# Optimization experiments

Measured on AMD Instinct MI355X. Metric: run time of the kernel, lower is better.

## Reference

```python
import jax, jax.numpy as jnp
import numpy as np

N = 50000        # num nodes
F = 64           # feature_size
G = 64           # graph_embedding_size
C = 4            # num_edge_cat
NNZ = 800000     # edges per category
L0 = 128         # first MLP hidden layer
EMB = 64         # embedding_size
EPS = 1e-5


def _glorot(key, shape):
    fan_in, fan_out = shape[-2], shape[-1]
    lim = jnp.sqrt(6.0 / (fan_in + fan_out))
    return jax.random.uniform(key, shape, jnp.float32, -lim, lim)


def setup_inputs() -> dict:
    key = jax.random.key(0)
    ks = jax.random.split(key, 8)
    A = jax.random.randint(ks[0], (C, 2, NNZ), 0, N, dtype=jnp.int64)
    X = jax.random.normal(ks[1], (N, F), jnp.float32)
    Ws = _glorot(ks[2], (C, F, G))            # per-edge-cat projection
    W0 = _glorot(ks[3], (C * G, L0))          # Linear0 weight (in,out)
    b0 = jnp.zeros((L0,), jnp.float32)
    gamma = jnp.ones((L0,), jnp.float32)      # BatchNorm1d weight
    beta = jnp.zeros((L0,), jnp.float32)      # BatchNorm1d bias
    W1 = _glorot(ks[4], (L0, EMB))            # Linear1 weight (in,out)
    b1 = jnp.zeros((EMB,), jnp.float32)
    return {"A": A, "X": X, "Ws": Ws, "W0": W0, "b0": b0,
            "gamma": gamma, "beta": beta, "W1": W1, "b1": b1,
            "mini_batch": 0}


def reference(A, X, Ws, W0, b0, gamma, beta, W1, b1, mini_batch):
    # mini_batch == False path. Instead of materializing dense NxN adjacency,
    # aggregate directly over edge lists (same math: (E @ X)[i] = sum_{(i,j) in E} X[j]).
    n = X.shape[0]
    XW = jnp.einsum('nf,cfg->cng', X, Ws)                       # [C,N,G]
    def agg(edges, xw):                                          # edges [2,nnz], xw [N,G]
        return jax.ops.segment_sum(xw[edges[1]], edges[0], num_segments=n)
    H = jax.vmap(agg)(A, XW)                                     # [C,N,G]
    H = jnp.transpose(H, (1, 0, 2)).reshape(n, -1)               # concat over edge cats -> [N, C*G]
    # NodeEmbedding: Linear -> BatchNorm1d (training stats) -> ELU -> Linear
    h = H @ W0 + b0
    mean = jnp.mean(h, axis=0)
    var = jnp.mean((h - mean) ** 2, axis=0)                      # biased var, as torch BN
    h = (h - mean) * jax.lax.rsqrt(var + EPS) * gamma + beta
    h = jax.nn.elu(h)
    return h @ W1 + b1                                           # [N, EMB]
```

## Files before the change

kernel.cpp:

```cpp
#include <hip/hip_runtime.h>
#include <hip/hip_bf16.h>

#define NN    50000
#define CC    4
#define NNZV  800000
#define TOTE  (CC * NNZV)
#define NWG   1024
#define EPW   (TOTE / NWG)
#define NFB   782
#define NPART 8
#define RCAPV 768
#define BCAP  (NPART * RCAPV)
#define NRB   782
#define NXB   782

using bf16 = __hip_bfloat16;
typedef short short8 __attribute__((ext_vector_type(8)));
typedef float f32x4  __attribute__((ext_vector_type(4)));
typedef unsigned short u16x8 __attribute__((ext_vector_type(8)));

__device__ __forceinline__ float bfu2f(unsigned short u) {
    union { unsigned int i; float f; } v;
    v.i = ((unsigned int)u) << 16;
    return v.f;
}
__device__ __forceinline__ float cvt(float x) { return x; }
__device__ __forceinline__ float cvt(bf16 x)  { return __bfloat162float(x); }
__device__ __forceinline__ unsigned short tobits(float x) {
    bf16 t = __float2bfloat16(x);
    return *(unsigned short*)&t;
}

__device__ __forceinline__ void detect_flags(const unsigned int* __restrict__ Xw,
                                             const unsigned int* __restrict__ Aw,
                                             int* dcnt, int& f32f, int& i64f) {
    const int t = threadIdx.x, nthr = blockDim.x;
    if (t < 2) dcnt[t] = 0;
    __syncthreads();
    int c1 = 0;
    for (int i = t; i < 1024; i += nthr) {
        unsigned b = (Xw[i] >> 7) & 0xFF;
        if (b >= 118 && b <= 134) c1++;
    }
    if (c1) atomicAdd(&dcnt[0], c1);
    if (t < 128) { if (Aw[2 * t + 1] == 0) atomicAdd(&dcnt[1], 1); }
    __syncthreads();
    f32f = (dcnt[0] < 512) ? 1 : 0;
    i64f = (dcnt[1] >= 96) ? 1 : 0;
    __syncthreads();
}

template<typename TF>
__device__ __forceinline__ void pack_body(const TF* __restrict__ W0, const TF* __restrict__ W1,
                                          const TF* __restrict__ Ws, const TF* __restrict__ b0,
                                          const TF* __restrict__ b1,
                                          unsigned short* __restrict__ Wb,
                                          unsigned short* __restrict__ Wb1,
                                          float* __restrict__ bias0, float* __restrict__ bias1,
                                          int trip) {
    const int lane = trip & 63;
    const int q = lane >> 4, cI = lane & 15;
    if (trip < 4096) {
        const int k0 = trip >> 9, t8 = (trip >> 6) & 7;
        const int kbase = k0 * 32 + q * 8;
        const int col   = t8 * 16 + cI;
        const int c     = kbase >> 6;
        float w0c[64];
        #pragma unroll
        for (int g = 0; g < 64; ++g)
            w0c[g] = cvt(W0[(size_t)(c * 64 + g) * 128 + col]);
        #pragma unroll
        for (int j = 0; j < 8; ++j) {
            const int f = (kbase + j) & 63;
            const TF* wsrow = Ws + ((size_t)c * 64 + f) * 64;
            float acc = 0.f;
            #pragma unroll
            for (int g = 0; g < 64; ++g)
                acc += cvt(wsrow[g]) * w0c[g];
            Wb[(size_t)trip * 8 + j] = tobits(acc);
        }
    } else if (trip < 5120) {
        const int u = trip - 4096;
        const int k0 = u >> 8, t4 = (u >> 6) & 3;
        #pragma unroll
        for (int j = 0; j < 8; ++j)
            Wb1[(size_t)u * 8 + j] =
                tobits(cvt(W1[(size_t)(k0 * 32 + q * 8 + j) * 64 + t4 * 16 + cI]));
    } else if (trip < 5248) {
        bias0[trip - 5120] = cvt(b0[trip - 5120]);
    } else if (trip < 5312) {
        bias1[trip - 5248] = cvt(b1[trip - 5248]);
    }
}

__global__ __launch_bounds__(256) void pack_kernel(const void* X, const void* A,
                                                   const void* W0, const void* W1,
                                                   const void* Ws, const void* b0,
                                                   const void* b1,
                                                   unsigned short* Wb, unsigned short* Wb1,
                                                   float* bias0, float* bias1,
                                                   unsigned int* zeroReg) {
    __shared__ int dcnt[2];
    int f32f, i64f;
    detect_flags((const unsigned int*)X, (const unsigned int*)A, dcnt, f32f, i64f);
    const int t = threadIdx.x;
    if (blockIdx.x == 0) {
        for (int i = t; i < 8448; i += 256) zeroReg[i] = 0u;
    }
    const int trip = blockIdx.x * 256 + t;
    if (trip >= 5312) return;
    if (f32f) pack_body<float>((const float*)W0, (const float*)W1, (const float*)Ws,
                               (const float*)b0, (const float*)b1, Wb, Wb1, bias0, bias1, trip);
    else      pack_body<bf16> ((const bf16*)W0, (const bf16*)W1, (const bf16*)Ws,
                               (const bf16*)b0, (const bf16*)b1, Wb, Wb1, bias0, bias1, trip);
}

template<typename TI>
__device__ __forceinline__ void cscat2_body(const TI* __restrict__ A,
                                            unsigned int* __restrict__ gcur,
                                            unsigned int* __restrict__ recs,
                                            unsigned int* lh, unsigned int* lrec) {
    const int w = blockIdx.x, t = threadIdx.x;
    const int v = w & (NPART - 1);
    #pragma unroll
    for (int u = 0; u < 4; ++u) lh[t + u * 256] = 0;
    __syncthreads();
    const int base   = w * EPW;
    const int c      = base / NNZV;
    const int eibase = base - c * NNZV;
    const TI* Ad = A + (size_t)(c * 2 + 0) * NNZV + eibase;
    const TI* As = A + (size_t)(c * 2 + 1) * NNZV + eibase;
    for (int i = t; i < EPW; i += 256) {
        const int dst = (int)Ad[i];
        const int src = (int)As[i];
        unsigned int rec = 0xFFFFFFFFu;
        if ((unsigned)dst < NN && (unsigned)src < NN) {
            rec = ((unsigned)dst << 16) | (unsigned)src;
            atomicAdd(&lh[dst >> 6], 1u);
        }
        lrec[i] = rec;
    }
    __syncthreads();
    unsigned int cl[4], sl[4];
    #pragma unroll
    for (int u = 0; u < 4; ++u) cl[u] = lh[t + u * 256];
    __syncthreads();
    #pragma unroll
    for (int u = 0; u < 4; ++u)
        sl[u] = cl[u] ? atomicAdd(&gcur[(v << 10) + t + u * 256], cl[u]) : 0u;
    #pragma unroll
    for (int u = 0; u < 4; ++u) lh[t + u * 256] = sl[u];
    __syncthreads();
    const unsigned int cb = (unsigned)c << 16;
    for (int i = t; i < EPW; i += 256) {
        const unsigned int rec = lrec[i];
        if (rec == 0xFFFFFFFFu) continue;
        const int dst = (int)(rec >> 16);
        const int b   = dst >> 6;
        const unsigned int pos = atomicAdd(&lh[b], 1u);
        if (pos < RCAPV)
            recs[((size_t)b * NPART + v) * RCAPV + pos] =
                ((unsigned)(dst & 63) << 18) | cb | (rec & 0xFFFFu);
    }
}

__device__ __forceinline__ void xconv_body(const void* __restrict__ X, int f32f,
                                           unsigned short* __restrict__ Xb, int bidx) {
    const size_t base = (size_t)bidx * 4096 + (size_t)threadIdx.x * 16;
    #pragma unroll
    for (int i = 0; i < 4; ++i) {
        const size_t off = base + (size_t)i * 4;
        if (off < (size_t)NN * 64) {
            ushort4 o;
            if (f32f) {
                const float4 v = *(const float4*)((const float*)X + off);
                o.x = tobits(v.x); o.y = tobits(v.y); o.z = tobits(v.z); o.w = tobits(v.w);
            } else {
                o = *(const ushort4*)((const unsigned short*)X + off);
            }
            *(ushort4*)(Xb + off) = o;
        } else if (off < (size_t)(NN + 1) * 64) {
            *(ushort4*)(Xb + off) = make_ushort4(0, 0, 0, 0);
        }
    }
}

__global__ __launch_bounds__(256) void fused_kernel(const void* __restrict__ X,
                                                    const void* __restrict__ A,
                                                    unsigned short* __restrict__ Xb,
                                                    unsigned int* __restrict__ gcur,
                                                    unsigned int* __restrict__ recs) {
    __shared__ unsigned int Su[1024 + EPW];
    __shared__ int dcnt[2];
    int f32f, i64f;
    detect_flags((const unsigned int*)X, (const unsigned int*)A, dcnt, f32f, i64f);
    if (blockIdx.x < NWG) {
        unsigned int* lh   = Su;
        unsigned int* lrec = Su + 1024;
        if (i64f) cscat2_body<long long>((const long long*)A, gcur, recs, lh, lrec);
        else      cscat2_body<int>      ((const int*)A,       gcur, recs, lh, lrec);
    } else {
        xconv_body(X, f32f, Xb, blockIdx.x - NWG);
    }
}

__global__ __launch_bounds__(512) void dgather_kernel(const unsigned int* __restrict__ gcur,
                                                      const unsigned int* __restrict__ recs,
                                                      const unsigned short* __restrict__ Xb,
                                                      unsigned short* __restrict__ S) {
    __shared__ unsigned short elist[8192];
    __shared__ unsigned int scnt[256], sstart[256], scur[256], send[256], ts[256];
    __shared__ unsigned int cntv[NPART];
    const int b = blockIdx.x, t = threadIdx.x;
    if (t < NPART) {
        unsigned int n = gcur[(t << 10) + b];
        cntv[t] = n < RCAPV ? n : RCAPV;
    }
    if (t < 256) scnt[t] = 0;
    __syncthreads();
    const size_t rb = (size_t)b * BCAP;
    #pragma unroll
    for (int v = 0; v < NPART; ++v) {
        const int n = (int)cntv[v];
        for (int i = t; i < n; i += 512)
            atomicAdd(&scnt[recs[rb + v * RCAPV + i] >> 16], 1u);
    }
    __syncthreads();
    unsigned int myp = 0;
    if (t < 256) { myp = (scnt[t] + 7u) & ~7u; ts[t] = myp; }
    __syncthreads();
    for (int off = 1; off < 256; off <<= 1) {
        unsigned int val = 0;
        if (t < 256 && t >= off) val = ts[t - off];
        __syncthreads();
        if (t < 256) ts[t] += val;
        __syncthreads();
    }
    if (t < 256) {
        const unsigned int ex = ts[t] - myp;
        sstart[t] = ex; scur[t] = ex; send[t] = ex + myp;
        for (unsigned int j = ex + scnt[t]; j < ex + myp; ++j)
            elist[j] = (unsigned short)NN;
    }
    __syncthreads();
    #pragma unroll
    for (int v = 0; v < NPART; ++v) {
        const int n = (int)cntv[v];
        for (int i = t; i < n; i += 512) {
            const unsigned int r = recs[rb + v * RCAPV + i];
            const unsigned int pos = atomicAdd(&scur[r >> 16], 1u);
            elist[pos] = (unsigned short)(r & 0xFFFFu);
        }
    }
    __syncthreads();
    const int g  = t >> 4;
    const int li = t & 15;
    const int g4 = li * 4;
    #pragma unroll
    for (int s8 = 0; s8 < 8; ++s8) {
        const int seg = g * 8 + s8;
        const int dst = b * 64 + (seg >> 2);
        const int c   = seg & 3;
        const int start = (int)sstart[seg];
        const int pcnt  = (int)(send[seg] - sstart[seg]);
        f32x4 acc = (f32x4){0.f, 0.f, 0.f, 0.f};
        if (pcnt > 0) {
            u16x8 idx = *(const u16x8*)(elist + start);
            for (int e0 = 0; e0 < pcnt; e0 += 8) {
                const u16x8 nidx = *(const u16x8*)(elist + start + e0 + 8);
                ushort4 v0 = *(const ushort4*)(Xb + (size_t)idx[0] * 64 + g4);
                ushort4 v1 = *(const ushort4*)(Xb + (size_t)idx[1] * 64 + g4);
                ushort4 v2 = *(const ushort4*)(Xb + (size_t)idx[2] * 64 + g4);
                ushort4 v3 = *(const ushort4*)(Xb + (size_t)idx[3] * 64 + g4);
                ushort4 v4 = *(const ushort4*)(Xb + (size_t)idx[4] * 64 + g4);
                ushort4 v5 = *(const ushort4*)(Xb + (size_t)idx[5] * 64 + g4);
                ushort4 v6 = *(const ushort4*)(Xb + (size_t)idx[6] * 64 + g4);
                ushort4 v7 = *(const ushort4*)(Xb + (size_t)idx[7] * 64 + g4);
                acc[0] += bfu2f(v0.x); acc[1] += bfu2f(v0.y); acc[2] += bfu2f(v0.z); acc[3] += bfu2f(v0.w);
                acc[0] += bfu2f(v1.x); acc[1] += bfu2f(v1.y); acc[2] += bfu2f(v1.z); acc[3] += bfu2f(v1.w);
                acc[0] += bfu2f(v2.x); acc[1] += bfu2f(v2.y); acc[2] += bfu2f(v2.z); acc[3] += bfu2f(v2.w);
                acc[0] += bfu2f(v3.x); acc[1] += bfu2f(v3.y); acc[2] += bfu2f(v3.z); acc[3] += bfu2f(v3.w);
                acc[0] += bfu2f(v4.x); acc[1] += bfu2f(v4.y); acc[2] += bfu2f(v4.z); acc[3] += bfu2f(v4.w);
                acc[0] += bfu2f(v5.x); acc[1] += bfu2f(v5.y); acc[2] += bfu2f(v5.z); acc[3] += bfu2f(v5.w);
                acc[0] += bfu2f(v6.x); acc[1] += bfu2f(v6.y); acc[2] += bfu2f(v6.z); acc[3] += bfu2f(v6.w);
                acc[0] += bfu2f(v7.x); acc[1] += bfu2f(v7.y); acc[2] += bfu2f(v7.z); acc[3] += bfu2f(v7.w);
                idx = nidx;
            }
        }
        if (dst < NN) {
            ushort4 o;
            o.x = tobits(acc[0]); o.y = tobits(acc[1]); o.z = tobits(acc[2]); o.w = tobits(acc[3]);
            *(ushort4*)(S + (size_t)dst * 256 + c * 64 + g4) = o;
        }
    }
}

__global__ __launch_bounds__(256) void l0_mfma(const unsigned short* __restrict__ Hg,
                                               const unsigned short* __restrict__ Wb,
                                               const float* __restrict__ bias0,
                                               unsigned short* __restrict__ hO,
                                               float* __restrict__ stats) {
    __shared__ unsigned short Hs[64 * 264];
    __shared__ float psum[128], psq[128];
    const int t = threadIdx.x;
    const int n0 = blockIdx.x * 64;
    #pragma unroll
    for (int i = 0; i < 16; ++i) {
        const int r = (t >> 6) + i * 4;
        const int k = (t & 63) * 4;
        const int row = n0 + r;
        ushort4 v = make_ushort4(0, 0, 0, 0);
        if (row < NN) v = *(const ushort4*)(Hg + (size_t)row * 256 + k);
        *(ushort4*)(&Hs[r * 264 + k]) = v;
    }
    if (t < 128) { psum[t] = 0.f; psq[t] = 0.f; }
    __syncthreads();
    const int w = t >> 6, lane = t & 63;
    const int q = lane >> 4, cI = lane & 15;
    f32x4 acc[8];
    #pragma unroll
    for (int i = 0; i < 8; ++i) acc[i] = (f32x4){0.f, 0.f, 0.f, 0.f};
    const unsigned short* arow = &Hs[(w * 16 + cI) * 264 + q * 8];
    #pragma unroll
    for (int k0 = 0; k0 < 8; ++k0) {
        short8 a = *(const short8*)(arow + k0 * 32);
        #pragma unroll
        for (int t8 = 0; t8 < 8; ++t8) {
            short8 b = *(const short8*)(Wb + ((size_t)(k0 * 8 + t8) * 64 + lane) * 8);
            acc[t8] = __builtin_amdgcn_mfma_f32_16x16x32_bf16(a, b, acc[t8], 0, 0, 0);
        }
    }
    __syncthreads();
    const int rloc  = w * 16 + q * 4;
    const int rbase = n0 + rloc;
    #pragma unroll
    for (int t8 = 0; t8 < 8; ++t8) {
        const int col = t8 * 16 + cI;
        const float bc = bias0[col];
        float s = 0.f, qq = 0.f;
        #pragma unroll
        for (int r = 0; r < 4; ++r) {
            float v = acc[t8][r] + bc;
            Hs[(rloc + r) * 136 + col] = tobits(v);
            if (rbase + r >= NN) v = 0.f;
            s += v; qq += v * v;
        }
        s  += __shfl_xor(s, 16, 64);  s  += __shfl_xor(s, 32, 64);
        qq += __shfl_xor(qq, 16, 64); qq += __shfl_xor(qq, 32, 64);
        if (q == 0) { atomicAdd(&psum[col], s); atomicAdd(&psq[col], qq); }
    }
    __syncthreads();
    if (t < 128) { atomicAdd(&stats[t], psum[t]); atomicAdd(&stats[128 + t], psq[t]); }
    #pragma unroll
    for (int i = 0; i < 4; ++i) {
        const int m    = t + i * 256;
        const int row  = m >> 4;
        const int col0 = (m & 15) * 8;
        const int grow = n0 + row;
        if (grow < NN) {
            *(ushort4*)(hO + (size_t)grow * 128 + col0)     = *(ushort4*)(&Hs[row * 136 + col0]);
            *(ushort4*)(hO + (size_t)grow * 128 + col0 + 4) = *(ushort4*)(&Hs[row * 136 + col0 + 4]);
        }
    }
}

__global__ __launch_bounds__(256) void l1_mfma(const void* __restrict__ X,
                                               const void* __restrict__ A,
                                               const unsigned short* __restrict__ hg,
                                               const float* __restrict__ stats,
                                               const void* __restrict__ gamma,
                                               const void* __restrict__ beta,
                                               const unsigned short* __restrict__ Wb1,
                                               const float* __restrict__ bias1,
                                               void* __restrict__ outv) {
    __shared__ unsigned short Es[64 * 136];
    __shared__ float coefL[256];
    __shared__ int dcnt[2];
    int f32f, i64f;
    detect_flags((const unsigned int*)X, (const unsigned int*)A, dcnt, f32f, i64f);
    const int t = threadIdx.x;
    if (t < 128) {
        const float invN = 1.0f / (float)NN;
        const float mean = stats[t] * invN;
        const float var  = stats[128 + t] * invN - mean * mean;
        const float inv  = rsqrtf(var + 1e-5f);
        const float ga = f32f ? ((const float*)gamma)[t] : cvt(((const bf16*)gamma)[t]);
        const float be = f32f ? ((const float*)beta)[t]  : cvt(((const bf16*)beta)[t]);
        const float a = ga * inv;
        coefL[t] = a;
        coefL[128 + t] = be - mean * a;
    }
    __syncthreads();
    const int n0 = blockIdx.x * 64;
    #pragma unroll
    for (int i = 0; i < 8; ++i) {
        const int r = (t >> 5) + i * 8;
        const int k = (t & 31) * 4;
        const int row = n0 + r;
        ushort4 o = make_ushort4(0, 0, 0, 0);
        if (row < NN) {
            ushort4 v = *(const ushort4*)(hg + (size_t)row * 128 + k);
            float f0 = coefL[k + 0] * bfu2f(v.x) + coefL[128 + k + 0];
            float f1 = coefL[k + 1] * bfu2f(v.y) + coefL[128 + k + 1];
            float f2 = coefL[k + 2] * bfu2f(v.z) + coefL[128 + k + 2];
            float f3 = coefL[k + 3] * bfu2f(v.w) + coefL[128 + k + 3];
            f0 = f0 > 0.f ? f0 : expm1f(f0);
            f1 = f1 > 0.f ? f1 : expm1f(f1);
            f2 = f2 > 0.f ? f2 : expm1f(f2);
            f3 = f3 > 0.f ? f3 : expm1f(f3);
            o.x = tobits(f0); o.y = tobits(f1); o.z = tobits(f2); o.w = tobits(f3);
        }
        *(ushort4*)(&Es[r * 136 + k]) = o;
    }
    __syncthreads();
    const int w = t >> 6, lane = t & 63;
    const int q = lane >> 4, cI = lane & 15;
    f32x4 acc[4];
    #pragma unroll
    for (int i = 0; i < 4; ++i) acc[i] = (f32x4){0.f, 0.f, 0.f, 0.f};
    const unsigned short* arow = &Es[(w * 16 + cI) * 136 + q * 8];
    #pragma unroll
    for (int k0 = 0; k0 < 4; ++k0) {
        short8 a = *(const short8*)(arow + k0 * 32);
        #pragma unroll
        for (int t4 = 0; t4 < 4; ++t4) {
            short8 b = *(const short8*)(Wb1 + ((size_t)(k0 * 4 + t4) * 64 + lane) * 8);
            acc[t4] = __builtin_amdgcn_mfma_f32_16x16x32_bf16(a, b, acc[t4], 0, 0, 0);
        }
    }
    __syncthreads();
    float* ot = (float*)Es;
    const int rloc = w * 16 + q * 4;
    #pragma unroll
    for (int t4 = 0; t4 < 4; ++t4) {
        const int col = t4 * 16 + cI;
        const float bc = bias1[col];
        #pragma unroll
        for (int r = 0; r < 4; ++r)
            ot[(rloc + r) * 68 + col] = acc[t4][r] + bc;
    }
    __syncthreads();
    #pragma unroll
    for (int i = 0; i < 4; ++i) {
        const int m    = t + i * 256;
        const int row  = m >> 4;
        const int col0 = (m & 15) * 4;
        const int grow = n0 + row;
        if (grow >= NN) continue;
        const float f0 = ot[row * 68 + col0 + 0];
        const float f1 = ot[row * 68 + col0 + 1];
        const float f2 = ot[row * 68 + col0 + 2];
        const float f3 = ot[row * 68 + col0 + 3];
        if (f32f) {
            float4 o; o.x = f0; o.y = f1; o.z = f2; o.w = f3;
            *(float4*)((float*)outv + (size_t)grow * 64 + col0) = o;
        } else {
            ushort4 o;
            o.x = tobits(f0); o.y = tobits(f1); o.z = tobits(f2); o.w = tobits(f3);
            *(ushort4*)((unsigned short*)outv + (size_t)grow * 64 + col0) = o;
        }
    }
}

extern "C" void kernel_launch(void* const* d_in, const int* in_sizes, int n_in,
                              void* d_out, int out_size, void* d_ws, size_t ws_size,
                              hipStream_t stream) {
    const void* A     = d_in[0];
    const void* X     = d_in[1];
    const void* Ws    = d_in[2];
    const void* W0    = d_in[3];
    const void* b0    = d_in[4];
    const void* gamma = d_in[5];
    const void* beta  = d_in[6];
    const void* W1    = d_in[7];
    const void* b1    = d_in[8];

    char* ws = (char*)d_ws;
    unsigned short* Xb       = (unsigned short*)(ws);
    unsigned short* S        = (unsigned short*)(ws + 6400256);
    unsigned short* h        = (unsigned short*)(ws + 32000256);
    unsigned int*   recs     = (unsigned int*)  (ws + 44800256);
    float*          stats    = (float*)         (ws + 64018688);
    unsigned int*   gcur     = (unsigned int*)  (ws + 64019712);
    unsigned short* Wb       = (unsigned short*)(ws + 64052480);
    unsigned short* Wb1      = (unsigned short*)(ws + 64118016);
    float*          bias0    = (float*)         (ws + 64134400);
    float*          bias1    = (float*)         (ws + 64134912);

    pack_kernel   <<<21, 256, 0, stream>>>(X, A, W0, W1, Ws, b0, b1,
                                           Wb, Wb1, bias0, bias1,
                                           (unsigned int*)stats );
    fused_kernel  <<<NWG + NXB, 256, 0, stream>>>(X, A, Xb, gcur, recs);
    dgather_kernel<<<NFB, 512, 0, stream>>>(gcur, recs, Xb, S);
    l0_mfma       <<<NRB, 256, 0, stream>>>(S, Wb, bias0, h, stats);
    l1_mfma       <<<NRB, 256, 0, stream>>>(X, A, h, stats, gamma, beta, Wb1, bias1, d_out);
}
```

Baseline: 236.3 us.

## Bucket edges per (dst,cat) segment via global atomics and fuse gather into L0

Replaces the two-level partitioned record scatter plus the separate dgather kernel with direct per-segment edge lists, built with one global atomic per edge into fixed-capacity slots. The neighbor gather now runs inside l0_mfma, writing aggregated rows straight into shared memory instead of materializing S in global memory. This removes one kernel launch and the S write/read round trip. In exchange it issues far more global atomics, caps each segment at 64 edges, and the zeroing of the much larger counter array in pack_kernel is spread over only 21 blocks.

```diff
diff --git a/kernel.cpp b/kernel.cpp
--- a/kernel.cpp
+++ b/kernel.cpp
@@ -7,10 +7,9 @@
 #define TOTE  (CC * NNZV)
 #define NWG   1024
 #define EPW   (TOTE / NWG)
-#define NFB   782
-#define NPART 8
-#define RCAPV 768
-#define BCAP  (NPART * RCAPV)
+#define NSEG  200000
+#define NSEGP 200704
+#define SCAP  64
 #define NRB   782
 #define NXB   782
 
@@ -104,9 +103,7 @@
     int f32f, i64f;
     detect_flags((const unsigned int*)X, (const unsigned int*)A, dcnt, f32f, i64f);
     const int t = threadIdx.x;
-    if (blockIdx.x == 0) {
-        for (int i = t; i < 8448; i += 256) zeroReg[i] = 0u;
-    }
+    for (int i = blockIdx.x * 256 + t; i < 200960; i += 21 * 256) zeroReg[i] = 0u;
     const int trip = blockIdx.x * 256 + t;
     if (trip >= 5312) return;
     if (f32f) pack_body<float>((const float*)W0, (const float*)W1, (const float*)Ws,
@@ -116,51 +113,23 @@
 }
 
 template<typename TI>
-__device__ __forceinline__ void cscat2_body(const TI* __restrict__ A,
-                                            unsigned int* __restrict__ gcur,
-                                            unsigned int* __restrict__ recs,
-                                            unsigned int* lh, unsigned int* lrec) {
+__device__ __forceinline__ void cscat_body(const TI* __restrict__ A,
+                                           unsigned int* __restrict__ segcnt,
+                                           unsigned short* __restrict__ elist) {
     const int w = blockIdx.x, t = threadIdx.x;
-    const int v = w & (NPART - 1);
-    #pragma unroll
-    for (int u = 0; u < 4; ++u) lh[t + u * 256] = 0;
-    __syncthreads();
-    const int base   = w * EPW;
-    const int c      = base / NNZV;
-    const int eibase = base - c * NNZV;
-    const TI* Ad = A + (size_t)(c * 2 + 0) * NNZV + eibase;
-    const TI* As = A + (size_t)(c * 2 + 1) * NNZV + eibase;
+    const int c   = w >> 8;
+    const int eib = (w & 255) * EPW;
+    const TI* Ad = A + (size_t)(c * 2 + 0) * NNZV + eib;
+    const TI* As = A + (size_t)(c * 2 + 1) * NNZV + eib;
     for (int i = t; i < EPW; i += 256) {
         const int dst = (int)Ad[i];
         const int src = (int)As[i];
-        unsigned int rec = 0xFFFFFFFFu;
         if ((unsigned)dst < NN && (unsigned)src < NN) {
-            rec = ((unsigned)dst << 16) | (unsigned)src;
-            atomicAdd(&lh[dst >> 6], 1u);
-        }
-        lrec[i] = rec;
-    }
-    __syncthreads();
-    unsigned int cl[4], sl[4];
-    #pragma unroll
-    for (int u = 0; u < 4; ++u) cl[u] = lh[t + u * 256];
-    __syncthreads();
-    #pragma unroll
-    for (int u = 0; u < 4; ++u)
-        sl[u] = cl[u] ? atomicAdd(&gcur[(v << 10) + t + u * 256], cl[u]) : 0u;
-    #pragma unroll
-    for (int u = 0; u < 4; ++u) lh[t + u * 256] = sl[u];
-    __syncthreads();
-    const unsigned int cb = (unsigned)c << 16;
-    for (int i = t; i < EPW; i += 256) {
-        const unsigned int rec = lrec[i];
-        if (rec == 0xFFFFFFFFu) continue;
-        const int dst = (int)(rec >> 16);
-        const int b   = dst >> 6;
-        const unsigned int pos = atomicAdd(&lh[b], 1u);
-        if (pos < RCAPV)
-            recs[((size_t)b * NPART + v) * RCAPV + pos] =
-                ((unsigned)(dst & 63) << 18) | cb | (rec & 0xFFFFu);
+            const int seg = dst * 4 + c;
+            const unsigned int pos = atomicAdd(&segcnt[seg], 1u);
+            if (pos < (unsigned)SCAP)
+                elist[(size_t)seg * SCAP + pos] = (unsigned short)src;
+        }
     }
 }
 
@@ -188,114 +157,22 @@
 __global__ __launch_bounds__(256) void fused_kernel(const void* __restrict__ X,
                                                     const void* __restrict__ A,
                                                     unsigned short* __restrict__ Xb,
-                                                    unsigned int* __restrict__ gcur,
-                                                    unsigned int* __restrict__ recs) {
-    __shared__ unsigned int Su[1024 + EPW];
+                                                    unsigned int* __restrict__ segcnt,
+                                                    unsigned short* __restrict__ elist) {
     __shared__ int dcnt[2];
     int f32f, i64f;
     detect_flags((const unsigned int*)X, (const unsigned int*)A, dcnt, f32f, i64f);
     if (blockIdx.x < NWG) {
-        unsigned int* lh   = Su;
-        unsigned int* lrec = Su + 1024;
-        if (i64f) cscat2_body<long long>((const long long*)A, gcur, recs, lh, lrec);
-        else      cscat2_body<int>      ((const int*)A,       gcur, recs, lh, lrec);
+        if (i64f) cscat_body<long long>((const long long*)A, segcnt, elist);
+        else      cscat_body<int>      ((const int*)A,       segcnt, elist);
     } else {
         xconv_body(X, f32f, Xb, blockIdx.x - NWG);
     }
 }
 
-__global__ __launch_bounds__(512) void dgather_kernel(const unsigned int* __restrict__ gcur,
-                                                      const unsigned int* __restrict__ recs,
-                                                      const unsigned short* __restrict__ Xb,
-                                                      unsigned short* __restrict__ S) {
-    __shared__ unsigned short elist[8192];
-    __shared__ unsigned int scnt[256], sstart[256], scur[256], send[256], ts[256];
-    __shared__ unsigned int cntv[NPART];
-    const int b = blockIdx.x, t = threadIdx.x;
-    if (t < NPART) {
-        unsigned int n = gcur[(t << 10) + b];
-        cntv[t] = n < RCAPV ? n : RCAPV;
-    }
-    if (t < 256) scnt[t] = 0;
-    __syncthreads();
-    const size_t rb = (size_t)b * BCAP;
-    #pragma unroll
-    for (int v = 0; v < NPART; ++v) {
-        const int n = (int)cntv[v];
-        for (int i = t; i < n; i += 512)
-            atomicAdd(&scnt[recs[rb + v * RCAPV + i] >> 16], 1u);
-    }
-    __syncthreads();
-    unsigned int myp = 0;
-    if (t < 256) { myp = (scnt[t] + 7u) & ~7u; ts[t] = myp; }
-    __syncthreads();
-    for (int off = 1; off < 256; off <<= 1) {
-        unsigned int val = 0;
-        if (t < 256 && t >= off) val = ts[t - off];
-        __syncthreads();
-        if (t < 256) ts[t] += val;
-        __syncthreads();
-    }
-    if (t < 256) {
-        const unsigned int ex = ts[t] - myp;
-        sstart[t] = ex; scur[t] = ex; send[t] = ex + myp;
-        for (unsigned int j = ex + scnt[t]; j < ex + myp; ++j)
-            elist[j] = (unsigned short)NN;
-    }
-    __syncthreads();
-    #pragma unroll
-    for (int v = 0; v < NPART; ++v) {
-        const int n = (int)cntv[v];
-        for (int i = t; i < n; i += 512) {
-            const unsigned int r = recs[rb + v * RCAPV + i];
-            const unsigned int pos = atomicAdd(&scur[r >> 16], 1u);
-            elist[pos] = (unsigned short)(r & 0xFFFFu);
-        }
-    }
-    __syncthreads();
-    const int g  = t >> 4;
-    const int li = t & 15;
-    const int g4 = li * 4;
-    #pragma unroll
-    for (int s8 = 0; s8 < 8; ++s8) {
-        const int seg = g * 8 + s8;
-        const int dst = b * 64 + (seg >> 2);
-        const int c   = seg & 3;
-        const int start = (int)sstart[seg];
-        const int pcnt  = (int)(send[seg] - sstart[seg]);
-        f32x4 acc = (f32x4){0.f, 0.f, 0.f, 0.f};
-        if (pcnt > 0) {
-            u16x8 idx = *(const u16x8*)(elist + start);
-            for (int e0 = 0; e0 < pcnt; e0 += 8) {
-                const u16x8 nidx = *(const u16x8*)(elist + start + e0 + 8);
-                ushort4 v0 = *(const ushort4*)(Xb + (size_t)idx[0] * 64 + g4);
-                ushort4 v1 = *(const ushort4*)(Xb + (size_t)idx[1] * 64 + g4);
-                ushort4 v2 = *(const ushort4*)(Xb + (size_t)idx[2] * 64 + g4);
-                ushort4 v3 = *(const ushort4*)(Xb + (size_t)idx[3] * 64 + g4);
-                ushort4 v4 = *(const ushort4*)(Xb + (size_t)idx[4] * 64 + g4);
-                ushort4 v5 = *(const ushort4*)(Xb + (size_t)idx[5] * 64 + g4);
-                ushort4 v6 = *(const ushort4*)(Xb + (size_t)idx[6] * 64 + g4);
-                ushort4 v7 = *(const ushort4*)(Xb + (size_t)idx[7] * 64 + g4);
-                acc[0] += bfu2f(v0.x); acc[1] += bfu2f(v0.y); acc[2] += bfu2f(v0.z); acc[3] += bfu2f(v0.w);
-                acc[0] += bfu2f(v1.x); acc[1] += bfu2f(v1.y); acc[2] += bfu2f(v1.z); acc[3] += bfu2f(v1.w);
-                acc[0] += bfu2f(v2.x); acc[1] += bfu2f(v2.y); acc[2] += bfu2f(v2.z); acc[3] += bfu2f(v2.w);
-                acc[0] += bfu2f(v3.x); acc[1] += bfu2f(v3.y); acc[2] += bfu2f(v3.z); acc[3] += bfu2f(v3.w);
-                acc[0] += bfu2f(v4.x); acc[1] += bfu2f(v4.y); acc[2] += bfu2f(v4.z); acc[3] += bfu2f(v4.w);
-                acc[0] += bfu2f(v5.x); acc[1] += bfu2f(v5.y); acc[2] += bfu2f(v5.z); acc[3] += bfu2f(v5.w);
-                acc[0] += bfu2f(v6.x); acc[1] += bfu2f(v6.y); acc[2] += bfu2f(v6.z); acc[3] += bfu2f(v6.w);
-                acc[0] += bfu2f(v7.x); acc[1] += bfu2f(v7.y); acc[2] += bfu2f(v7.z); acc[3] += bfu2f(v7.w);
-                idx = nidx;
-            }
-        }
-        if (dst < NN) {
-            ushort4 o;
-            o.x = tobits(acc[0]); o.y = tobits(acc[1]); o.z = tobits(acc[2]); o.w = tobits(acc[3]);
-            *(ushort4*)(S + (size_t)dst * 256 + c * 64 + g4) = o;
-        }
-    }
-}
-
-__global__ __launch_bounds__(256) void l0_mfma(const unsigned short* __restrict__ Hg,
+__global__ __launch_bounds__(256) void l0_mfma(const unsigned short* __restrict__ elist,
+                                               const unsigned int* __restrict__ segcnt,
+                                               const unsigned short* __restrict__ Xb,
                                                const unsigned short* __restrict__ Wb,
                                                const float* __restrict__ bias0,
                                                unsigned short* __restrict__ hO,
@@ -304,16 +181,66 @@
     __shared__ float psum[128], psq[128];
     const int t = threadIdx.x;
     const int n0 = blockIdx.x * 64;
-    #pragma unroll
-    for (int i = 0; i < 16; ++i) {
-        const int r = (t >> 6) + i * 4;
-        const int k = (t & 63) * 4;
-        const int row = n0 + r;
-        ushort4 v = make_ushort4(0, 0, 0, 0);
-        if (row < NN) v = *(const ushort4*)(Hg + (size_t)row * 256 + k);
-        *(ushort4*)(&Hs[r * 264 + k]) = v;
-    }
+    const int g  = t >> 4;
+    const int li = t & 15;
+    const int g4 = li * 4;
+    const int gl = (t >> 4) & 3;
+    const int segb = (n0 + g * 4) * 4;
+    const unsigned int mycnt = segcnt[segb + li];
     if (t < 128) { psum[t] = 0.f; psq[t] = 0.f; }
+    for (int s = 0; s < 16; ++s) {
+        unsigned int cnt = __shfl(mycnt, gl * 16 + s, 64);
+        if (cnt > (unsigned)SCAP) cnt = SCAP;
+        const int r = g * 4 + (s >> 2);
+        const int c = s & 3;
+        const unsigned short* ep = elist + (size_t)(segb + s) * SCAP;
+        f32x4 acc = (f32x4){0.f, 0.f, 0.f, 0.f};
+        int e0 = 0;
+        for (; e0 + 8 <= (int)cnt; e0 += 8) {
+            const u16x8 idx = *(const u16x8*)(ep + e0);
+            ushort4 v0 = *(const ushort4*)(Xb + (size_t)idx[0] * 64 + g4);
+            ushort4 v1 = *(const ushort4*)(Xb + (size_t)idx[1] * 64 + g4);
+            ushort4 v2 = *(const ushort4*)(Xb + (size_t)idx[2] * 64 + g4);
+            ushort4 v3 = *(const ushort4*)(Xb + (size_t)idx[3] * 64 + g4);
+            ushort4 v4 = *(const ushort4*)(Xb + (size_t)idx[4] * 64 + g4);
+            ushort4 v5 = *(const ushort4*)(Xb + (size_t)idx[5] * 64 + g4);
+            ushort4 v6 = *(const ushort4*)(Xb + (size_t)idx[6] * 64 + g4);
+            ushort4 v7 = *(const ushort4*)(Xb + (size_t)idx[7] * 64 + g4);
+            acc[0] += bfu2f(v0.x); acc[1] += bfu2f(v0.y); acc[2] += bfu2f(v0.z); acc[3] += bfu2f(v0.w);
+            acc[0] += bfu2f(v1.x); acc[1] += bfu2f(v1.y); acc[2] += bfu2f(v1.z); acc[3] += bfu2f(v1.w);
+            acc[0] += bfu2f(v2.x); acc[1] += bfu2f(v2.y); acc[2] += bfu2f(v2.z); acc[3] += bfu2f(v2.w);
+            acc[0] += bfu2f(v3.x); acc[1] += bfu2f(v3.y); acc[2] += bfu2f(v3.z); acc[3] += bfu2f(v3.w);
+            acc[0] += bfu2f(v4.x); acc[1] += bfu2f(v4.y); acc[2] += bfu2f(v4.z); acc[3] += bfu2f(v4.w);
+            acc[0] += bfu2f(v5.x); acc[1] += bfu2f(v5.y); acc[2] += bfu2f(v5.z); acc[3] += bfu2f(v5.w);
+            acc[0] += bfu2f(v6.x); acc[1] += bfu2f(v6.y); acc[2] += bfu2f(v6.z); acc[3] += bfu2f(v6.w);
+            acc[0] += bfu2f(v7.x); acc[1] += bfu2f(v7.y); acc[2] += bfu2f(v7.z); acc[3] += bfu2f(v7.w);
+        }
+        if (e0 < (int)cnt) {
+            u16x8 idx = *(const u16x8*)(ep + e0);
+            #pragma unroll
+            for (int j = 0; j < 8; ++j)
+                idx[j] = (e0 + j < (int)cnt) ? idx[j] : (unsigned short)NN;
+            ushort4 v0 = *(const ushort4*)(Xb + (size_t)idx[0] * 64 + g4);
+            ushort4 v1 = *(const ushort4*)(Xb + (size_t)idx[1] * 64 + g4);
+            ushort4 v2 = *(const ushort4*)(Xb + (size_t)idx[2] * 64 + g4);
+            ushort4 v3 = *(const ushort4*)(Xb + (size_t)idx[3] * 64 + g4);
+            ushort4 v4 = *(const ushort4*)(Xb + (size_t)idx[4] * 64 + g4);
+            ushort4 v5 = *(const ushort4*)(Xb + (size_t)idx[5] * 64 + g4);
+            ushort4 v6 = *(const ushort4*)(Xb + (size_t)idx[6] * 64 + g4);
+            ushort4 v7 = *(const ushort4*)(Xb + (size_t)idx[7] * 64 + g4);
+            acc[0] += bfu2f(v0.x); acc[1] += bfu2f(v0.y); acc[2] += bfu2f(v0.z); acc[3] += bfu2f(v0.w);
+            acc[0] += bfu2f(v1.x); acc[1] += bfu2f(v1.y); acc[2] += bfu2f(v1.z); acc[3] += bfu2f(v1.w);
+            acc[0] += bfu2f(v2.x); acc[1] += bfu2f(v2.y); acc[2] += bfu2f(v2.z); acc[3] += bfu2f(v2.w);
+            acc[0] += bfu2f(v3.x); acc[1] += bfu2f(v3.y); acc[2] += bfu2f(v3.z); acc[3] += bfu2f(v3.w);
+            acc[0] += bfu2f(v4.x); acc[1] += bfu2f(v4.y); acc[2] += bfu2f(v4.z); acc[3] += bfu2f(v4.w);
+            acc[0] += bfu2f(v5.x); acc[1] += bfu2f(v5.y); acc[2] += bfu2f(v5.z); acc[3] += bfu2f(v5.w);
+            acc[0] += bfu2f(v6.x); acc[1] += bfu2f(v6.y); acc[2] += bfu2f(v6.z); acc[3] += bfu2f(v6.w);
+            acc[0] += bfu2f(v7.x); acc[1] += bfu2f(v7.y); acc[2] += bfu2f(v7.z); acc[3] += bfu2f(v7.w);
+        }
+        ushort4 o;
+        o.x = tobits(acc[0]); o.y = tobits(acc[1]); o.z = tobits(acc[2]); o.w = tobits(acc[3]);
+        *(ushort4*)(&Hs[r * 264 + c * 64 + g4]) = o;
+    }
     __syncthreads();
     const int w = t >> 6, lane = t & 63;
     const int q = lane >> 4, cI = lane & 15;
@@ -477,21 +404,19 @@
 
     char* ws = (char*)d_ws;
     unsigned short* Xb       = (unsigned short*)(ws);
-    unsigned short* S        = (unsigned short*)(ws + 6400256);
-    unsigned short* h        = (unsigned short*)(ws + 32000256);
-    unsigned int*   recs     = (unsigned int*)  (ws + 44800256);
-    float*          stats    = (float*)         (ws + 64018688);
-    unsigned int*   gcur     = (unsigned int*)  (ws + 64019712);
-    unsigned short* Wb       = (unsigned short*)(ws + 64052480);
-    unsigned short* Wb1      = (unsigned short*)(ws + 64118016);
-    float*          bias0    = (float*)         (ws + 64134400);
-    float*          bias1    = (float*)         (ws + 64134912);
-
-    pack_kernel   <<<21, 256, 0, stream>>>(X, A, W0, W1, Ws, b0, b1,
-                                           Wb, Wb1, bias0, bias1,
-                                           (unsigned int*)stats );
-    fused_kernel  <<<NWG + NXB, 256, 0, stream>>>(X, A, Xb, gcur, recs);
-    dgather_kernel<<<NFB, 512, 0, stream>>>(gcur, recs, Xb, S);
-    l0_mfma       <<<NRB, 256, 0, stream>>>(S, Wb, bias0, h, stats);
-    l1_mfma       <<<NRB, 256, 0, stream>>>(X, A, h, stats, gamma, beta, Wb1, bias1, d_out);
-}
+    unsigned short* h        = (unsigned short*)(ws + 6400256);
+    unsigned short* elist    = (unsigned short*)(ws + 19200256);
+    float*          stats    = (float*)         (ws + 44800256);
+    unsigned int*   segcnt   = (unsigned int*)  (ws + 44801280);
+    unsigned short* Wb       = (unsigned short*)(ws + 45604096);
+    unsigned short* Wb1      = (unsigned short*)(ws + 45669632);
+    float*          bias0    = (float*)         (ws + 45686016);
+    float*          bias1    = (float*)         (ws + 45686528);
+
+    pack_kernel <<<21, 256, 0, stream>>>(X, A, W0, W1, Ws, b0, b1,
+                                         Wb, Wb1, bias0, bias1,
+                                         (unsigned int*)stats );
+    fused_kernel<<<NWG + NXB, 256, 0, stream>>>(X, A, Xb, segcnt, elist);
+    l0_mfma     <<<NRB, 256, 0, stream>>>(elist, segcnt, Xb, Wb, bias0, h, stats);
+    l1_mfma     <<<NRB, 256, 0, stream>>>(X, A, h, stats, gamma, beta, Wb1, bias1, d_out);
+}
```

After: 345.3 us. +46.1%, slower.

## Fuse gather aggregation into the first MLP layer kernel via shared memory

Applied to the files above, without the earlier changes.

The destination-bucketed gather is merged into the first linear-layer MFMA kernel. Aggregated rows are written straight into a shared-memory tile instead of a global intermediate S, which removes a 25.6 MB write and read-back plus one kernel launch. The MFMA stage now runs with 512 threads: 8 waves, each covering a 16-row by 64-column quarter. Shared memory per block grows (elist plus Hs), which may reduce occupancy for the gather phase.

```diff
diff --git a/kernel.cpp b/kernel.cpp
--- a/kernel.cpp
+++ b/kernel.cpp
@@ -204,19 +204,26 @@
     }
 }
 
-__global__ __launch_bounds__(512) void dgather_kernel(const unsigned int* __restrict__ gcur,
-                                                      const unsigned int* __restrict__ recs,
-                                                      const unsigned short* __restrict__ Xb,
-                                                      unsigned short* __restrict__ S) {
+__global__ __launch_bounds__(512) void l0_mfma(const unsigned int* __restrict__ gcur,
+                                               const unsigned int* __restrict__ recs,
+                                               const unsigned short* __restrict__ Xb,
+                                               const unsigned short* __restrict__ Wb,
+                                               const float* __restrict__ bias0,
+                                               unsigned short* __restrict__ hO,
+                                               float* __restrict__ stats) {
     __shared__ unsigned short elist[8192];
+    __shared__ unsigned short Hs[64 * 264];
     __shared__ unsigned int scnt[256], sstart[256], scur[256], send[256], ts[256];
     __shared__ unsigned int cntv[NPART];
+    __shared__ float psum[128], psq[128];
     const int b = blockIdx.x, t = threadIdx.x;
+    const int n0 = b * 64;
     if (t < NPART) {
         unsigned int n = gcur[(t << 10) + b];
         cntv[t] = n < RCAPV ? n : RCAPV;
     }
     if (t < 256) scnt[t] = 0;
+    if (t < 128) { psum[t] = 0.f; psq[t] = 0.f; }
     __syncthreads();
     const size_t rb = (size_t)b * BCAP;
     #pragma unroll
@@ -253,94 +260,76 @@
         }
     }
     __syncthreads();
-    const int g  = t >> 4;
-    const int li = t & 15;
-    const int g4 = li * 4;
-    #pragma unroll
-    for (int s8 = 0; s8 < 8; ++s8) {
-        const int seg = g * 8 + s8;
-        const int dst = b * 64 + (seg >> 2);
-        const int c   = seg & 3;
-        const int start = (int)sstart[seg];
-        const int pcnt  = (int)(send[seg] - sstart[seg]);
-        f32x4 acc = (f32x4){0.f, 0.f, 0.f, 0.f};
-        if (pcnt > 0) {
-            u16x8 idx = *(const u16x8*)(elist + start);
-            for (int e0 = 0; e0 < pcnt; e0 += 8) {
-                const u16x8 nidx = *(const u16x8*)(elist + start + e0 + 8);
-                ushort4 v0 = *(const ushort4*)(Xb + (size_t)idx[0] * 64 + g4);
-                ushort4 v1 = *(const ushort4*)(Xb + (size_t)idx[1] * 64 + g4);
-                ushort4 v2 = *(const ushort4*)(Xb + (size_t)idx[2] * 64 + g4);
-                ushort4 v3 = *(const ushort4*)(Xb + (size_t)idx[3] * 64 + g4);
-                ushort4 v4 = *(const ushort4*)(Xb + (size_t)idx[4] * 64 + g4);
-                ushort4 v5 = *(const ushort4*)(Xb + (size_t)idx[5] * 64 + g4);
-                ushort4 v6 = *(const ushort4*)(Xb + (size_t)idx[6] * 64 + g4);
-                ushort4 v7 = *(const ushort4*)(Xb + (size_t)idx[7] * 64 + g4);
-                acc[0] += bfu2f(v0.x); acc[1] += bfu2f(v0.y); acc[2] += bfu2f(v0.z); acc[3] += bfu2f(v0.w);
-                acc[0] += bfu2f(v1.x); acc[1] += bfu2f(v1.y); acc[2] += bfu2f(v1.z); acc[3] += bfu2f(v1.w);
-                acc[0] += bfu2f(v2.x); acc[1] += bfu2f(v2.y); acc[2] += bfu2f(v2.z); acc[3] += bfu2f(v2.w);
-                acc[0] += bfu2f(v3.x); acc[1] += bfu2f(v3.y); acc[2] += bfu2f(v3.z); acc[3] += bfu2f(v3.w);
-                acc[0] += bfu2f(v4.x); acc[1] += bfu2f(v4.y); acc[2] += bfu2f(v4.z); acc[3] += bfu2f(v4.w);
-                acc[0] += bfu2f(v5.x); acc[1] += bfu2f(v5.y); acc[2] += bfu2f(v5.z); acc[3] += bfu2f(v5.w);
-                acc[0] += bfu2f(v6.x); acc[1] += bfu2f(v6.y); acc[2] += bfu2f(v6.z); acc[3] += bfu2f(v6.w);
-                acc[0] += bfu2f(v7.x); acc[1] += bfu2f(v7.y); acc[2] += bfu2f(v7.z); acc[3] += bfu2f(v7.w);
-                idx = nidx;
+    {
+        const int g  = t >> 4;
+        const int li = t & 15;
+        const int g4 = li * 4;
+        #pragma unroll
+        for (int s8 = 0; s8 < 8; ++s8) {
+            const int seg = g * 8 + s8;
+            const int row = seg >> 2;
+            const int c   = seg & 3;
+            const int start = (int)sstart[seg];
+            const int pcnt  = (int)(send[seg] - sstart[seg]);
+            f32x4 acc = (f32x4){0.f, 0.f, 0.f, 0.f};
+            if (pcnt > 0) {
+                u16x8 idx = *(const u16x8*)(elist + start);
+                for (int e0 = 0; e0 < pcnt; e0 += 8) {
+                    const u16x8 nidx = *(const u16x8*)(elist + start + e0 + 8);
+                    ushort4 v0 = *(const ushort4*)(Xb + (size_t)idx[0] * 64 + g4);
+                    ushort4 v1 = *(const ushort4*)(Xb + (size_t)idx[1] * 64 + g4);
+                    ushort4 v2 = *(const ushort4*)(Xb + (size_t)idx[2] * 64 + g4);
+                    ushort4 v3 = *(const ushort4*)(Xb + (size_t)idx[3] * 64 + g4);
+                    ushort4 v4 = *(const ushort4*)(Xb + (size_t)idx[4] * 64 + g4);
+                    ushort4 v5 = *(const ushort4*)(Xb + (size_t)idx[5] * 64 + g4);
+                    ushort4 v6 = *(const ushort4*)(Xb + (size_t)idx[6] * 64 + g4);
+                    ushort4 v7 = *(const ushort4*)(Xb + (size_t)idx[7] * 64 + g4);
+                    acc[0] += bfu2f(v0.x); acc[1] += bfu2f(v0.y); acc[2] += bfu2f(v0.z); acc[3] += bfu2f(v0.w);
+                    acc[0] += bfu2f(v1.x); acc[1] += bfu2f(v1.y); acc[2] += bfu2f(v1.z); acc[3] += bfu2f(v1.w);
+                    acc[0] += bfu2f(v2.x); acc[1] += bfu2f(v2.y); acc[2] += bfu2f(v2.z); acc[3] += bfu2f(v2.w);
+                    acc[0] += bfu2f(v3.x); acc[1] += bfu2f(v3.y); acc[2] += bfu2f(v3.z); acc[3] += bfu2f(v3.w);
+                    acc[0] += bfu2f(v4.x); acc[1] += bfu2f(v4.y); acc[2] += bfu2f(v4.z); acc[3] += bfu2f(v4.w);
+                    acc[0] += bfu2f(v5.x); acc[1] += bfu2f(v5.y); acc[2] += bfu2f(v5.z); acc[3] += bfu2f(v5.w);
+                    acc[0] += bfu2f(v6.x); acc[1] += bfu2f(v6.y); acc[2] += bfu2f(v6.z); acc[3] += bfu2f(v6.w);
+                    acc[0] += bfu2f(v7.x); acc[1] += bfu2f(v7.y); acc[2] += bfu2f(v7.z); acc[3] += bfu2f(v7.w);
+                    idx = nidx;
+                }
             }
-        }
-        if (dst < NN) {
             ushort4 o;
             o.x = tobits(acc[0]); o.y = tobits(acc[1]); o.z = tobits(acc[2]); o.w = tobits(acc[3]);
-            *(ushort4*)(S + (size_t)dst * 256 + c * 64 + g4) = o;
-        }
-    }
-}
-
-__global__ __launch_bounds__(256) void l0_mfma(const unsigned short* __restrict__ Hg,
-                                               const unsigned short* __restrict__ Wb,
-                                               const float* __restrict__ bias0,
-                                               unsigned short* __restrict__ hO,
-                                               float* __restrict__ stats) {
-    __shared__ unsigned short Hs[64 * 264];
-    __shared__ float psum[128], psq[128];
-    const int t = threadIdx.x;
-    const int n0 = blockIdx.x * 64;
-    #pragma unroll
-    for (int i = 0; i < 16; ++i) {
-        const int r = (t >> 6) + i * 4;
-        const int k = (t & 63) * 4;
-        const int row = n0 + r;
-        ushort4 v = make_ushort4(0, 0, 0, 0);
-        if (row < NN) v = *(const ushort4*)(Hg + (size_t)row * 256 + k);
-        *(ushort4*)(&Hs[r * 264 + k]) = v;
-    }
-    if (t < 128) { psum[t] = 0.f; psq[t] = 0.f; }
+            *(ushort4*)(&Hs[row * 264 + c * 64 + g4]) = o;
+        }
+    }
     __syncthreads();
     const int w = t >> 6, lane = t & 63;
     const int q = lane >> 4, cI = lane & 15;
-    f32x4 acc[8];
-    #pragma unroll
-    for (int i = 0; i < 8; ++i) acc[i] = (f32x4){0.f, 0.f, 0.f, 0.f};
-    const unsigned short* arow = &Hs[(w * 16 + cI) * 264 + q * 8];
+    const int wr = w & 3;
+    const int wc = w >> 2;
+    f32x4 acc[4];
+    #pragma unroll
+    for (int i = 0; i < 4; ++i) acc[i] = (f32x4){0.f, 0.f, 0.f, 0.f};
+    const unsigned short* arow = &Hs[(wr * 16 + cI) * 264 + q * 8];
     #pragma unroll
     for (int k0 = 0; k0 < 8; ++k0) {
         short8 a = *(const short8*)(arow + k0 * 32);
         #pragma unroll
-        for (int t8 = 0; t8 < 8; ++t8) {
-            short8 b = *(const short8*)(Wb + ((size_t)(k0 * 8 + t8) * 64 + lane) * 8);
-            acc[t8] = __builtin_amdgcn_mfma_f32_16x16x32_bf16(a, b, acc[t8], 0, 0, 0);
-        }
-    }
-    __syncthreads();
-    const int rloc  = w * 16 + q * 4;
+        for (int t4 = 0; t4 < 4; ++t4) {
+            const int t8 = wc * 4 + t4;
+            short8 bb = *(const short8*)(Wb + ((size_t)(k0 * 8 + t8) * 64 + lane) * 8);
+            acc[t4] = __builtin_amdgcn_mfma_f32_16x16x32_bf16(a, bb, acc[t4], 0, 0, 0);
+        }
+    }
+    __syncthreads();
+    const int rloc  = wr * 16 + q * 4;
     const int rbase = n0 + rloc;
     #pragma unroll
-    for (int t8 = 0; t8 < 8; ++t8) {
-        const int col = t8 * 16 + cI;
+    for (int t4 = 0; t4 < 4; ++t4) {
+        const int col = (wc * 4 + t4) * 16 + cI;
         const float bc = bias0[col];
         float s = 0.f, qq = 0.f;
         #pragma unroll
         for (int r = 0; r < 4; ++r) {
-            float v = acc[t8][r] + bc;
+            float v = acc[t4][r] + bc;
             Hs[(rloc + r) * 136 + col] = tobits(v);
             if (rbase + r >= NN) v = 0.f;
             s += v; qq += v * v;
@@ -352,8 +341,8 @@
     __syncthreads();
     if (t < 128) { atomicAdd(&stats[t], psum[t]); atomicAdd(&stats[128 + t], psq[t]); }
     #pragma unroll
-    for (int i = 0; i < 4; ++i) {
-        const int m    = t + i * 256;
+    for (int i = 0; i < 2; ++i) {
+        const int m    = t + i * 512;
         const int row  = m >> 4;
         const int col0 = (m & 15) * 8;
         const int grow = n0 + row;
@@ -477,21 +466,19 @@
 
     char* ws = (char*)d_ws;
     unsigned short* Xb       = (unsigned short*)(ws);
-    unsigned short* S        = (unsigned short*)(ws + 6400256);
-    unsigned short* h        = (unsigned short*)(ws + 32000256);
-    unsigned int*   recs     = (unsigned int*)  (ws + 44800256);
-    float*          stats    = (float*)         (ws + 64018688);
-    unsigned int*   gcur     = (unsigned int*)  (ws + 64019712);
-    unsigned short* Wb       = (unsigned short*)(ws + 64052480);
-    unsigned short* Wb1      = (unsigned short*)(ws + 64118016);
-    float*          bias0    = (float*)         (ws + 64134400);
-    float*          bias1    = (float*)         (ws + 64134912);
-
-    pack_kernel   <<<21, 256, 0, stream>>>(X, A, W0, W1, Ws, b0, b1,
-                                           Wb, Wb1, bias0, bias1,
-                                           (unsigned int*)stats );
-    fused_kernel  <<<NWG + NXB, 256, 0, stream>>>(X, A, Xb, gcur, recs);
-    dgather_kernel<<<NFB, 512, 0, stream>>>(gcur, recs, Xb, S);
-    l0_mfma       <<<NRB, 256, 0, stream>>>(S, Wb, bias0, h, stats);
-    l1_mfma       <<<NRB, 256, 0, stream>>>(X, A, h, stats, gamma, beta, Wb1, bias1, d_out);
-}
+    unsigned short* h        = (unsigned short*)(ws + 6400256);
+    unsigned int*   recs     = (unsigned int*)  (ws + 19200256);
+    float*          stats    = (float*)         (ws + 38418688);
+    unsigned int*   gcur     = (unsigned int*)  (ws + 38419712);
+    unsigned short* Wb       = (unsigned short*)(ws + 38452480);
+    unsigned short* Wb1      = (unsigned short*)(ws + 38518016);
+    float*          bias0    = (float*)         (ws + 38534400);
+    float*          bias1    = (float*)         (ws + 38534912);
+
+    pack_kernel <<<21, 256, 0, stream>>>(X, A, W0, W1, Ws, b0, b1,
+                                         Wb, Wb1, bias0, bias1,
+                                         (unsigned int*)stats );
+    fused_kernel<<<NWG + NXB, 256, 0, stream>>>(X, A, Xb, gcur, recs);
+    l0_mfma     <<<NRB, 512, 0, stream>>>(gcur, recs, Xb, Wb, bias0, h, stats);
+    l1_mfma     <<<NRB, 256, 0, stream>>>(X, A, h, stats, gamma, beta, Wb1, bias1, d_out);
+}
```

New measurement: 225.8 us. -4.5%, faster.
